# Kernel tuning notes

Measured on AMD Instinct MI355X. Metric: run time of the kernel, lower is better.

## Reference

```python
import jax, jax.numpy as jnp
import numpy as np

SS = 25.0 / 255.0   # spatial_scale = 1 / (SEARCH_SIZE/25), SEARCH_SIZE = 255
OUT = 7             # ROIPOOL_OUTSIZE // 4, ROIPOOL_OUTSIZE = 28
SP = 4              # sample_per_part (mmdet DeformRoIPooling default)
TRANS_STD = 0.1


def _deform_roi_pool(x, rois, offset):
    # x: [B,C,H,W]; rois: [N,5] (batch_idx,x1,y1,x2,y2); offset: [N,2,OUT,OUT] (ch0=x, ch1=y)
    B, C, H, W = x.shape
    N = rois.shape[0]
    b = rois[:, 0].astype(jnp.int32)
    sw = jnp.round(rois[:, 1]) * SS - 0.5
    sh = jnp.round(rois[:, 2]) * SS - 0.5
    rw = jnp.maximum((jnp.round(rois[:, 3]) + 1.0) * SS - 0.5 - sw, 0.1)
    rh = jnp.maximum((jnp.round(rois[:, 4]) + 1.0) * SS - 0.5 - sh, 0.1)
    bw, bh = rw / OUT, rh / OUT
    p = jnp.arange(OUT, dtype=x.dtype)
    tx = offset[:, 0] * TRANS_STD  # [N,OUT,OUT] indexed [n,ph,pw]
    ty = offset[:, 1] * TRANS_STD
    wstart = p[None, None, :] * bw[:, None, None] + sw[:, None, None] + tx * rw[:, None, None]
    hstart = p[None, :, None] * bh[:, None, None] + sh[:, None, None] + ty * rh[:, None, None]
    s = jnp.arange(SP, dtype=x.dtype)
    # sample coords [N,OUT,OUT,SP(ih),SP(iw)]
    sx = wstart[..., None, None] + s[None, None, None, None, :] * (bw / SP)[:, None, None, None, None]
    sy = hstart[..., None, None] + s[None, None, None, :, None] * (bh / SP)[:, None, None, None, None]
    valid = (sx >= -0.5) & (sx <= W - 0.5) & (sy >= -0.5) & (sy <= H - 0.5)
    xc = jnp.clip(sx, 0.0, W - 1.0)
    yc = jnp.clip(sy, 0.0, H - 1.0)
    x0 = jnp.floor(xc)
    y0 = jnp.floor(yc)
    dx = xc - x0
    dy = yc - y0
    xi0 = x0.astype(jnp.int32)
    yi0 = y0.astype(jnp.int32)
    xi1 = jnp.ceil(xc).astype(jnp.int32)
    yi1 = jnp.ceil(yc).astype(jnp.int32)
    feat = jnp.transpose(x, (0, 2, 3, 1))  # [B,H,W,C]
    bb = b[:, None, None, None, None]

    def g(yi, xi):
        return feat[bb, yi, xi]  # [N,OUT,OUT,SP,SP,C]

    val = (((1 - dx) * (1 - dy))[..., None] * g(yi0, xi0)
           + (dx * (1 - dy))[..., None] * g(yi0, xi1)
           + ((1 - dx) * dy)[..., None] * g(yi1, xi0)
           + (dx * dy)[..., None] * g(yi1, xi1))
    val = jnp.where(valid[..., None], val, 0.0)
    cnt = valid.sum(axis=(3, 4)).astype(x.dtype)              # [N,OUT,OUT]
    pooled = val.sum(axis=(3, 4)) / jnp.maximum(cnt, 1.0)[..., None]
    return jnp.transpose(pooled, (0, 3, 1, 2))                # [N,C,OUT,OUT]


def _lin(h, w, b):
    return h @ w.T + b


def _forward(x, rois, off_w1, off_b1, off_w2, off_b2, off_w3, off_b3,
             fc1_w, fc1_b, fc2_w, fc2_b, box_w, box_b):
    N = rois.shape[0]
    zero_off = jnp.zeros((N, 2, OUT, OUT), x.dtype)
    # pass 1: no-trans pooling -> offset prediction
    p0 = _deform_roi_pool(x, rois, zero_off).reshape(N, -1)
    h = jax.nn.relu(_lin(p0, off_w1, off_b1))
    h = jax.nn.relu(_lin(h, off_w2, off_b2))
    off = _lin(h, off_w3, off_b3).reshape(N, 2, OUT, OUT)
    # pass 2: deformable pooling with predicted offsets
    p = _deform_roi_pool(x, rois, off).reshape(N, -1)
    h = jax.nn.relu(_lin(p, fc1_w, fc1_b))
    h = jax.nn.relu(_lin(h, fc2_w, fc2_b))
    return _lin(h, box_w, box_b)  # [N,4]


def setup_inputs():
    key = jax.random.key(0)
    ks = jax.random.split(key, 16)
    B, C, H, W, N = 8, 256, 25, 25, 256
    IN = C * OUT * OUT  # 12544
    DFC, FCC = 1024, 512
    x = jax.random.normal(ks[0], (B, C, H, W), jnp.float32)
    bidx = jax.random.randint(ks[1], (N,), 0, B).astype(jnp.float32)
    x1 = jax.random.uniform(ks[2], (N,), minval=0.0, maxval=180.0)
    y1 = jax.random.uniform(ks[3], (N,), minval=0.0, maxval=180.0)
    wd = jax.random.uniform(ks[4], (N,), minval=24.0, maxval=120.0)
    ht = jax.random.uniform(ks[5], (N,), minval=24.0, maxval=120.0)
    rois = jnp.stack([bidx, x1, y1, jnp.clip(x1 + wd, 0.0, 254.0),
                      jnp.clip(y1 + ht, 0.0, 254.0)], axis=1)

    def lin_p(k, o, i):
        return jax.random.normal(k, (o, i), jnp.float32) * (1.0 / np.sqrt(i))

    return dict(
        x=x, rois=rois,
        off_w1=lin_p(ks[6], DFC, IN), off_b1=jnp.zeros((DFC,), jnp.float32),
        off_w2=lin_p(ks[7], DFC, DFC), off_b2=jnp.zeros((DFC,), jnp.float32),
        off_w3=lin_p(ks[8], 2 * OUT * OUT, DFC) * 0.1,
        off_b3=jnp.zeros((2 * OUT * OUT,), jnp.float32),
        fc1_w=lin_p(ks[9], FCC, IN), fc1_b=jnp.zeros((FCC,), jnp.float32),
        fc2_w=lin_p(ks[10], FCC, FCC), fc2_b=jnp.zeros((FCC,), jnp.float32),
        box_w=lin_p(ks[11], 4, FCC) * 0.001, box_b=jnp.zeros((4,), jnp.float32),
    )


def reference(x, rois, off_w1, off_b1, off_w2, off_b2, off_w3, off_b3,
              fc1_w, fc1_b, fc2_w, fc2_b, box_w, box_b):
    return _forward(x, rois, off_w1, off_b1, off_w2, off_b2, off_w3, off_b3,
                    fc1_w, fc1_b, fc2_w, fc2_b, box_w, box_b)
```

## Files before the change

kernel.cpp:

```cpp
#include <hip/hip_runtime.h>
#include <hip/hip_bf16.h>


#define NROI 256
#define NB   8
#define INF  12544
#define DFC  1024
#define FCC  512

typedef __attribute__((ext_vector_type(8))) short short8;
typedef __attribute__((ext_vector_type(4))) float floatx4;

static __device__ __forceinline__ unsigned short f2bf(float f) {
    unsigned int u = __float_as_uint(f);
    unsigned int r = (u + 0x7fffu + ((u >> 16) & 1u)) >> 16;
    return (unsigned short)r;
}

static __device__ __forceinline__ void async_copy16(const void* g, void* l) {
    __builtin_amdgcn_global_load_lds(
        (const __attribute__((address_space(1))) unsigned int*)g,
        (__attribute__((address_space(3))) unsigned int*)l, 16, 0, 0);
}

__global__ __launch_bounds__(256) void transpose_kernel(
        const float* __restrict__ x, float* __restrict__ xT) {
    __shared__ float t[32][33];
    int b  = blockIdx.z;
    int cb = blockIdx.y * 32;
    int lb = blockIdx.x * 32;
    int tx = threadIdx.x & 31, ty = threadIdx.x >> 5;
#pragma unroll
    for (int r = 0; r < 4; ++r) {
        int c = cb + ty + r * 8, l = lb + tx;
        if (l < 625) t[ty + r * 8][tx] = x[(size_t)(b * 256 + c) * 625 + l];
    }
    __syncthreads();
#pragma unroll
    for (int r = 0; r < 4; ++r) {
        int l = lb + ty + r * 8, c = cb + tx;
        if (l < 625) xT[((size_t)b * 625 + l) * 256 + c] = t[tx][ty + r * 8];
    }
}

__global__ __launch_bounds__(256) void pool_prep(
        const float* __restrict__ rois, const float* __restrict__ off, int has_off,
        float* __restrict__ wbuf, int* __restrict__ bbuf) {
    __shared__ float g[256][16];
    const float SSC = (float)(25.0 / 255.0);
    int tid = threadIdx.x;
    int idx = blockIdx.x * 256 + tid;
    int n = idx / 49;
    int bin = idx - n * 49;
    const float* r = rois + n * 5;
    int b = (int)r[0];
    float sw = rintf(r[1]) * SSC - 0.5f;
    float sh = rintf(r[2]) * SSC - 0.5f;
    float rw = fmaxf((rintf(r[3]) + 1.0f) * SSC - 0.5f - sw, 0.1f);
    float rh = fmaxf((rintf(r[4]) + 1.0f) * SSC - 0.5f - sh, 0.1f);
    float bw = rw / 7.0f, bh = rh / 7.0f;
    float bws = bw * 0.25f, bhs = bh * 0.25f;
    int ph = bin / 7, pw = bin - ph * 7;
    float tx = 0.f, ty = 0.f;
    if (has_off) {
        tx = off[n * 98 + bin] * 0.1f;
        ty = off[n * 98 + 49 + bin] * 0.1f;
    }
    float wstart = pw * bw + sw + tx * rw;
    float hstart = ph * bh + sh + ty * rh;
#pragma unroll
    for (int i = 0; i < 16; ++i) g[tid][i] = 0.f;
    int gy0 = 0, gx0 = 0, cnt = 0;
#pragma unroll
    for (int s = 0; s < 16; ++s) {
        float fx = wstart + (s & 3) * bws;
        float fy = hstart + (s >> 2) * bhs;
        bool valid = (fx >= -0.5f) && (fx <= 24.5f) && (fy >= -0.5f) && (fy <= 24.5f);
        float xc = fminf(fmaxf(fx, 0.f), 24.f);
        float yc = fminf(fmaxf(fy, 0.f), 24.f);
        float x0f = floorf(xc), y0f = floorf(yc);
        float dx = xc - x0f, dy = yc - y0f;
        int x0 = (int)x0f, y0 = (int)y0f;
        int x1 = (int)ceilf(xc), y1 = (int)ceilf(yc);
        if (s == 0) { gy0 = y0; gx0 = x0; }
        float w00 = (1.f - dx) * (1.f - dy), w01 = dx * (1.f - dy);
        float w10 = (1.f - dx) * dy,         w11 = dx * dy;
        if (!valid) { w00 = w01 = w10 = w11 = 0.f; }
        cnt += valid ? 1 : 0;
        int ry0 = (y0 - gy0) * 4, ry1 = (y1 - gy0) * 4;
        g[tid][ry0 + (x0 - gx0)] += w00;
        g[tid][ry0 + (x1 - gx0)] += w01;
        g[tid][ry1 + (x0 - gx0)] += w10;
        g[tid][ry1 + (x1 - gx0)] += w11;
    }
    float inv = 1.0f / fmaxf((float)cnt, 1.0f);
    float4* wp = (float4*)(wbuf + (size_t)idx * 16);
#pragma unroll
    for (int q = 0; q < 4; ++q)
        wp[q] = make_float4(g[tid][q * 4] * inv, g[tid][q * 4 + 1] * inv,
                            g[tid][q * 4 + 2] * inv, g[tid][q * 4 + 3] * inv);
    bbuf[idx] = gy0 | (gx0 << 8) | (b << 16);
}

__global__ __launch_bounds__(256) void pool_gather(
        const float* __restrict__ feat, const float* __restrict__ wbuf,
        const int* __restrict__ bbuf, unsigned short* __restrict__ P) {
    __shared__ unsigned short sOut[128 * 49];
    int q = blockIdx.x;
    int n = blockIdx.y;
    int tid = threadIdx.x;
    int wv = tid >> 6, lane = tid & 63;
    int cbase = q * 128 + lane * 2;

    for (int bin = wv; bin < 49; bin += 4) {
        int di = n * 49 + bin;
        int base = bbuf[di];
        int gy0 = base & 255, gx0 = (base >> 8) & 255, b = base >> 16;
        const float4* wp = (const float4*)(wbuf + (size_t)di * 16);
        float4 w0 = wp[0], w1 = wp[1], w2 = wp[2], w3 = wp[3];
        float ww[16] = { w0.x, w0.y, w0.z, w0.w, w1.x, w1.y, w1.z, w1.w,
                         w2.x, w2.y, w2.z, w2.w, w3.x, w3.y, w3.z, w3.w };
        int rowOff[4], colOff[4];
#pragma unroll
        for (int r = 0; r < 4; ++r) {
            rowOff[r] = min(gy0 + r, 24) * 25;
            colOff[r] = min(gx0 + r, 24);
        }
        int b625 = b * 625;
        float ax = 0.f, ay = 0.f;
#pragma unroll
        for (int cell = 0; cell < 16; ++cell) {
            int pix = b625 + rowOff[cell >> 2] + colOff[cell & 3];
            float2 v = *(const float2*)(feat + (size_t)pix * 256 + cbase);
            ax += ww[cell] * v.x;
            ay += ww[cell] * v.y;
        }
        sOut[(lane * 2) * 49 + bin] = f2bf(ax);
        sOut[(lane * 2 + 1) * 49 + bin] = f2bf(ay);
    }
    __syncthreads();
    const uint2* so = (const uint2*)sOut;
    uint2* dp = (uint2*)(P + (size_t)n * INF + q * 128 * 49);
    for (int i = tid; i < 128 * 49 / 4; i += 256) dp[i] = so[i];
}

template <int BN>
__global__ __launch_bounds__(256) void gemm_nt_part(
        const unsigned short* __restrict__ A, const float* __restrict__ Bw,
        float* __restrict__ Cpart, int N, int K, int kSteps) {
    constexpr int BM = 256;
    constexpr int LDB = 40;
    __shared__ unsigned short As[BM * 32];
    __shared__ unsigned short Bs[BN * LDB];
    const int tid = threadIdx.x;
    const int lane = tid & 63;
    const int wave = tid >> 6;
    const int n0 = blockIdx.x * BN;
    const int k0 = blockIdx.z * kSteps * 32;
    const int quad = lane >> 4;
    const int l16 = lane & 15;
    constexpr int FM = 4, FN = BN / 16;

    floatx4 acc[FM][FN];
#pragma unroll
    for (int i = 0; i < FM; ++i)
#pragma unroll
        for (int j = 0; j < FN; ++j) acc[i][j] = (floatx4)0.f;

    const unsigned short* agp[4];
    void* alp[4];
#pragma unroll
    for (int i = 0; i < 4; ++i) {
        int idx = tid + i * 256;
        int row = idx >> 2;
        int qq = (idx & 3) ^ ((row >> 1) & 3);
        agp[i] = A + (size_t)row * K + qq * 8;
        alp[i] = (char*)As + ((size_t)i * 256 + wave * 64) * 16;
    }
    const int brow = tid >> 3, bq = tid & 7;
    const float* bgp = Bw + (size_t)(n0 + brow) * K + bq * 4;
    unsigned short* blp = Bs + brow * LDB + bq * 4;

    float4 bv = *(const float4*)(bgp + k0);
    for (int ks = 0; ks < kSteps; ++ks) {
        int kk = k0 + ks * 32;
        __syncthreads();
#pragma unroll
        for (int i = 0; i < 4; ++i)
            async_copy16(agp[i] + kk, alp[i]);
        {
            ushort4 h;
            h.x = f2bf(bv.x); h.y = f2bf(bv.y); h.z = f2bf(bv.z); h.w = f2bf(bv.w);
            *(ushort4*)blp = h;
        }
        if (ks + 1 < kSteps) bv = *(const float4*)(bgp + kk + 32);
        __syncthreads();
        short8 a[FM], bfr[FN];
#pragma unroll
        for (int i = 0; i < FM; ++i) {
            int r = wave * 64 + i * 16 + l16;
            int slot = quad ^ ((r >> 1) & 3);
            a[i] = *(const short8*)(As + r * 32 + slot * 8);
        }
#pragma unroll
        for (int j = 0; j < FN; ++j)
            bfr[j] = *(const short8*)(Bs + (j * 16 + l16) * LDB + quad * 8);
#pragma unroll
        for (int i = 0; i < FM; ++i)
#pragma unroll
            for (int j = 0; j < FN; ++j)
                acc[i][j] = __builtin_amdgcn_mfma_f32_16x16x32_bf16(a[i], bfr[j], acc[i][j], 0, 0, 0);
    }
    float* Cp = Cpart + (size_t)blockIdx.z * BM * N;
#pragma unroll
    for (int i = 0; i < FM; ++i)
#pragma unroll
        for (int rr = 0; rr < 4; ++rr) {
            int row = wave * 64 + i * 16 + quad * 4 + rr;
            float* cr = Cp + (size_t)row * N + n0;
#pragma unroll
            for (int j = 0; j < FN; ++j)
                cr[j * 16 + l16] = acc[i][j][rr];
        }
}

__global__ __launch_bounds__(256) void reduce_bias(
        const float* __restrict__ part, int zc, int mn4,
        const float* __restrict__ bias, int nmask, int relu,
        unsigned short* __restrict__ obf, float* __restrict__ of) {
    int idx = blockIdx.x * 256 + threadIdx.x;
    if (idx >= mn4) return;
    int idx4 = idx * 4;
    const float* bp = bias + (idx4 & nmask);
    float4 acc = *(const float4*)bp;
    const float4* p = (const float4*)part + idx;
    for (int z = 0; z < zc; ++z) {
        float4 v = p[(size_t)z * mn4];
        acc.x += v.x; acc.y += v.y; acc.z += v.z; acc.w += v.w;
    }
    if (relu) {
        acc.x = fmaxf(acc.x, 0.f); acc.y = fmaxf(acc.y, 0.f);
        acc.z = fmaxf(acc.z, 0.f); acc.w = fmaxf(acc.w, 0.f);
    }
    if (obf) {
        ushort4 h;
        h.x = f2bf(acc.x); h.y = f2bf(acc.y); h.z = f2bf(acc.z); h.w = f2bf(acc.w);
        *(ushort4*)(obf + idx4) = h;
    }
    if (of) *(float4*)(of + idx4) = acc;
}

__global__ __launch_bounds__(128) void fc_small(
        const float* __restrict__ h2, const float* __restrict__ w3,
        const float* __restrict__ b3, float* __restrict__ out) {
    __shared__ float shl[1024];
    int n = blockIdx.x, tid = threadIdx.x;
    for (int i = tid; i < 1024; i += 128) shl[i] = fmaxf(h2[(size_t)n * 1024 + i], 0.f);
    __syncthreads();
    if (tid < 98) {
        float acc = b3[tid];
        const float* w = w3 + (size_t)tid * 1024;
        for (int k = 0; k < 1024; k += 4) {
            float4 wv = *(const float4*)(w + k);
            acc += shl[k] * wv.x + shl[k + 1] * wv.y + shl[k + 2] * wv.z + shl[k + 3] * wv.w;
        }
        out[n * 98 + tid] = acc;
    }
}

__global__ __launch_bounds__(64) void head_kernel(
        const float* __restrict__ h4, const float* __restrict__ bw,
        const float* __restrict__ bb, float* __restrict__ out) {
    int n = blockIdx.x, t = threadIdx.x;
    float a0 = 0, a1 = 0, a2 = 0, a3 = 0;
    for (int k = t; k < 512; k += 64) {
        float v = fmaxf(h4[(size_t)n * 512 + k], 0.f);
        a0 += v * bw[k]; a1 += v * bw[512 + k];
        a2 += v * bw[1024 + k]; a3 += v * bw[1536 + k];
    }
#pragma unroll
    for (int o = 32; o > 0; o >>= 1) {
        a0 += __shfl_down(a0, o); a1 += __shfl_down(a1, o);
        a2 += __shfl_down(a2, o); a3 += __shfl_down(a3, o);
    }
    if (t == 0) {
        out[n * 4 + 0] = a0 + bb[0]; out[n * 4 + 1] = a1 + bb[1];
        out[n * 4 + 2] = a2 + bb[2]; out[n * 4 + 3] = a3 + bb[3];
    }
}

extern "C" void kernel_launch(void* const* d_in, const int* in_sizes, int n_in,
                              void* d_out, int out_size, void* d_ws, size_t ws_size,
                              hipStream_t stream) {
    const float* x      = (const float*)d_in[0];
    const float* rois   = (const float*)d_in[1];
    const float* off_w1 = (const float*)d_in[2];
    const float* off_b1 = (const float*)d_in[3];
    const float* off_w2 = (const float*)d_in[4];
    const float* off_b2 = (const float*)d_in[5];
    const float* off_w3 = (const float*)d_in[6];
    const float* off_b3 = (const float*)d_in[7];
    const float* fc1_w  = (const float*)d_in[8];
    const float* fc1_b  = (const float*)d_in[9];
    const float* fc2_w  = (const float*)d_in[10];
    const float* fc2_b  = (const float*)d_in[11];
    const float* box_w  = (const float*)d_in[12];
    const float* box_b  = (const float*)d_in[13];
    float* out = (float*)d_out;

    char* ws = (char*)d_ws;
    size_t o = 0;
    auto carve = [&](size_t bytes) { char* p = ws + o; o += (bytes + 255) & ~(size_t)255; return p; };
    float*          xT   = (float*)carve((size_t)NB * 625 * 256 * 4);
    unsigned short* P    = (unsigned short*)carve((size_t)NROI * INF * 2);
    unsigned short* h1b  = (unsigned short*)carve((size_t)NROI * DFC * 2);
    float*          h2   = (float*)carve((size_t)NROI * DFC * 4);
    float*          offb = (float*)carve((size_t)NROI * 98 * 4);
    unsigned short* h3b  = (unsigned short*)carve((size_t)NROI * FCC * 2);
    float*          h4   = (float*)carve((size_t)NROI * FCC * 4);
    float*          wbuf = (float*)carve((size_t)NROI * 49 * 16 * 4);
    int*            bbuf = (int*)carve((size_t)NROI * 49 * 4);
    size_t fixed = o;
    const size_t SLAB = (size_t)NROI * DFC * 4;
    int zg1;
    if      (ws_size >= fixed + 28 * SLAB) zg1 = 28;
    else if (ws_size >= fixed + 14 * SLAB) zg1 = 14;
    else                                   zg1 = 7;
    int zg2 = (zg1 >= 8) ? 8 : 4;
    float* part = (float*)carve((size_t)zg1 * SLAB);

    transpose_kernel<<<dim3(20, 8, 8), 256, 0, stream>>>(x, xT);
    pool_prep<<<49, 256, 0, stream>>>(rois, nullptr, 0, wbuf, bbuf);
    pool_gather<<<dim3(2, NROI), 256, 0, stream>>>(xT, wbuf, bbuf, P);
    gemm_nt_part<32><<<dim3(32, 1, zg1), 256, 0, stream>>>(P, off_w1, part, DFC, INF, 392 / zg1);
    reduce_bias<<<256, 256, 0, stream>>>(part, zg1, NROI * DFC / 4, off_b1, DFC - 1, 1, h1b, nullptr);
    gemm_nt_part<32><<<dim3(32, 1, zg2), 256, 0, stream>>>(h1b, off_w2, part, DFC, DFC, 32 / zg2);
    reduce_bias<<<256, 256, 0, stream>>>(part, zg2, NROI * DFC / 4, off_b2, DFC - 1, 0, nullptr, h2);
    fc_small<<<NROI, 128, 0, stream>>>(h2, off_w3, off_b3, offb);
    pool_prep<<<49, 256, 0, stream>>>(rois, offb, 1, wbuf, bbuf);
    pool_gather<<<dim3(2, NROI), 256, 0, stream>>>(xT, wbuf, bbuf, P);
    gemm_nt_part<32><<<dim3(16, 1, zg1), 256, 0, stream>>>(P, fc1_w, part, FCC, INF, 392 / zg1);
    reduce_bias<<<128, 256, 0, stream>>>(part, zg1, NROI * FCC / 4, fc1_b, FCC - 1, 1, h3b, nullptr);
    gemm_nt_part<32><<<dim3(16, 1, zg2), 256, 0, stream>>>(h3b, fc2_w, part, FCC, FCC, 16 / zg2);
    reduce_bias<<<128, 256, 0, stream>>>(part, zg2, NROI * FCC / 4, fc2_b, FCC - 1, 0, nullptr, h4);
    head_kernel<<<NROI, 64, 0, stream>>>(h4, box_w, box_b, out);
}
```

Baseline: 315.5 us.

## Load GEMM fragments directly from global into registers, dropping LDS staging

The split-K GEMM no longer stages A and B tiles through shared memory with async copies and barriers. Each lane now loads its MFMA fragments straight from global memory into registers, prefetching one k-step ahead, and converts B from fp32 to bf16 in registers. Launch bounds now request two blocks per CU. This removes the LDS traffic and the __syncthreads calls, but each B element is now loaded and converted by all four waves instead of once per block, and the A and B loads are strided 16-byte accesses rather than coalesced tile loads.

```diff
diff --git a/kernel.cpp b/kernel.cpp
--- a/kernel.cpp
+++ b/kernel.cpp
@@ -15,12 +15,6 @@
     unsigned int u = __float_as_uint(f);
     unsigned int r = (u + 0x7fffu + ((u >> 16) & 1u)) >> 16;
     return (unsigned short)r;
-}
-
-static __device__ __forceinline__ void async_copy16(const void* g, void* l) {
-    __builtin_amdgcn_global_load_lds(
-        (const __attribute__((address_space(1))) unsigned int*)g,
-        (__attribute__((address_space(3))) unsigned int*)l, 16, 0, 0);
 }
 
 __global__ __launch_bounds__(256) void transpose_kernel(
@@ -145,13 +139,11 @@
 }
 
 template <int BN>
-__global__ __launch_bounds__(256) void gemm_nt_part(
+__global__ __launch_bounds__(256, 2) void gemm_nt_part(
         const unsigned short* __restrict__ A, const float* __restrict__ Bw,
         float* __restrict__ Cpart, int N, int K, int kSteps) {
     constexpr int BM = 256;
-    constexpr int LDB = 40;
-    __shared__ unsigned short As[BM * 32];
-    __shared__ unsigned short Bs[BN * LDB];
+    constexpr int FM = 4, FN = BN / 16;
     const int tid = threadIdx.x;
     const int lane = tid & 63;
     const int wave = tid >> 6;
@@ -159,7 +151,6 @@
     const int k0 = blockIdx.z * kSteps * 32;
     const int quad = lane >> 4;
     const int l16 = lane & 15;
-    constexpr int FM = 4, FN = BN / 16;
 
     floatx4 acc[FM][FN];
 #pragma unroll
@@ -167,49 +158,56 @@
 #pragma unroll
         for (int j = 0; j < FN; ++j) acc[i][j] = (floatx4)0.f;
 
-    const unsigned short* agp[4];
-    void* alp[4];
-#pragma unroll
-    for (int i = 0; i < 4; ++i) {
-        int idx = tid + i * 256;
-        int row = idx >> 2;
-        int qq = (idx & 3) ^ ((row >> 1) & 3);
-        agp[i] = A + (size_t)row * K + qq * 8;
-        alp[i] = (char*)As + ((size_t)i * 256 + wave * 64) * 16;
-    }
-    const int brow = tid >> 3, bq = tid & 7;
-    const float* bgp = Bw + (size_t)(n0 + brow) * K + bq * 4;
-    unsigned short* blp = Bs + brow * LDB + bq * 4;
-
-    float4 bv = *(const float4*)(bgp + k0);
+    const unsigned short* ap[FM];
+#pragma unroll
+    for (int i = 0; i < FM; ++i)
+        ap[i] = A + (size_t)(wave * 64 + i * 16 + l16) * K + k0 + quad * 8;
+    const float* bp[FN];
+#pragma unroll
+    for (int j = 0; j < FN; ++j)
+        bp[j] = Bw + (size_t)(n0 + j * 16 + l16) * K + k0 + quad * 8;
+
+    short8 an[FM];
+    float4 bn0[FN], bn1[FN];
+#pragma unroll
+    for (int i = 0; i < FM; ++i) an[i] = *(const short8*)ap[i];
+#pragma unroll
+    for (int j = 0; j < FN; ++j) {
+        bn0[j] = *(const float4*)bp[j];
+        bn1[j] = *(const float4*)(bp[j] + 4);
+    }
+
     for (int ks = 0; ks < kSteps; ++ks) {
-        int kk = k0 + ks * 32;
-        __syncthreads();
-#pragma unroll
-        for (int i = 0; i < 4; ++i)
-            async_copy16(agp[i] + kk, alp[i]);
-        {
-            ushort4 h;
-            h.x = f2bf(bv.x); h.y = f2bf(bv.y); h.z = f2bf(bv.z); h.w = f2bf(bv.w);
-            *(ushort4*)blp = h;
-        }
-        if (ks + 1 < kSteps) bv = *(const float4*)(bgp + kk + 32);
-        __syncthreads();
-        short8 a[FM], bfr[FN];
-#pragma unroll
-        for (int i = 0; i < FM; ++i) {
-            int r = wave * 64 + i * 16 + l16;
-            int slot = quad ^ ((r >> 1) & 3);
-            a[i] = *(const short8*)(As + r * 32 + slot * 8);
-        }
-#pragma unroll
-        for (int j = 0; j < FN; ++j)
-            bfr[j] = *(const short8*)(Bs + (j * 16 + l16) * LDB + quad * 8);
-#pragma unroll
-        for (int i = 0; i < FM; ++i)
-#pragma unroll
-            for (int j = 0; j < FN; ++j)
-                acc[i][j] = __builtin_amdgcn_mfma_f32_16x16x32_bf16(a[i], bfr[j], acc[i][j], 0, 0, 0);
+        short8 a[FM];
+        float4 b0[FN], b1[FN];
+#pragma unroll
+        for (int i = 0; i < FM; ++i) a[i] = an[i];
+#pragma unroll
+        for (int j = 0; j < FN; ++j) { b0[j] = bn0[j]; b1[j] = bn1[j]; }
+        if (ks + 1 < kSteps) {
+#pragma unroll
+            for (int i = 0; i < FM; ++i) {
+                ap[i] += 32;
+                an[i] = *(const short8*)ap[i];
+            }
+#pragma unroll
+            for (int j = 0; j < FN; ++j) {
+                bp[j] += 32;
+                bn0[j] = *(const float4*)bp[j];
+                bn1[j] = *(const float4*)(bp[j] + 4);
+            }
+        }
+#pragma unroll
+        for (int j = 0; j < FN; ++j) {
+            short8 bf;
+            bf[0] = (short)f2bf(b0[j].x); bf[1] = (short)f2bf(b0[j].y);
+            bf[2] = (short)f2bf(b0[j].z); bf[3] = (short)f2bf(b0[j].w);
+            bf[4] = (short)f2bf(b1[j].x); bf[5] = (short)f2bf(b1[j].y);
+            bf[6] = (short)f2bf(b1[j].z); bf[7] = (short)f2bf(b1[j].w);
+#pragma unroll
+            for (int i = 0; i < FM; ++i)
+                acc[i][j] = __builtin_amdgcn_mfma_f32_16x16x32_bf16(a[i], bf, acc[i][j], 0, 0, 0);
+        }
     }
     float* Cp = Cpart + (size_t)blockIdx.z * BM * N;
 #pragma unroll
```

After: 338.5 us. 1.07x slower.
